# Performance work log

Measured on AMD Instinct MI355X. Metric: run time of the kernel, lower is better.

## Reference

```python
import jax, jax.numpy as jnp
import numpy as np

N_HEAD = 12

def setup_inputs() -> dict:
    key = jax.random.key(0)
    k1, k2, k3 = jax.random.split(key, 3)
    nx = 768
    B, S = 2, 2048
    return {
        "hidden_states": jax.random.normal(k1, (B, S, nx), dtype=jnp.float32),
        "w_attn": jax.random.normal(k2, (nx, 3 * nx), dtype=jnp.float32) * 0.02,
        "b_attn": jnp.zeros((3 * nx,), dtype=jnp.float32),
        "w_proj": jax.random.normal(k3, (nx, nx), dtype=jnp.float32) * 0.02,
        "b_proj": jnp.zeros((nx,), dtype=jnp.float32),
    }

def reference(hidden_states, w_attn, b_attn, w_proj, b_proj):
    B, S, nx = hidden_states.shape
    d_head = nx // N_HEAD
    qkv = hidden_states @ w_attn + b_attn  # [B,S,3nx]
    q, k, v = jnp.split(qkv, 3, axis=-1)
    # split heads -> [B,H,S,d]
    def split(x):
        return x.reshape(B, S, N_HEAD, d_head).transpose(0, 2, 1, 3)
    q, k, v = split(q), split(k), split(v)
    # scale=True: divide by sqrt(d_head) (v.size(-1))
    w = jnp.einsum("bhsd,bhtd->bhst", q, k) / jnp.sqrt(jnp.float32(d_head))
    w = jax.nn.softmax(w, axis=-1)
    a = jnp.einsum("bhst,bhtd->bhsd", w, v)  # [B,H,S,d]
    a = a.transpose(0, 2, 1, 3).reshape(B, S, nx)  # merge heads
    return a @ w_proj + b_proj
```

## Files before the change

kernel.cpp:

```cpp
#include <hip/hip_runtime.h>

#define NHEAD 12
#define DHEAD 64
#define SEQ   2048
#define NB    2
#define NX    768
#define MTOK  (NB * SEQ)

typedef __attribute__((ext_vector_type(8))) short short8;
typedef __attribute__((ext_vector_type(4))) short short4v;
typedef __attribute__((ext_vector_type(4))) float f32x4;

__device__ __forceinline__ unsigned short f2bf(float x) {
    union { float f; unsigned u; } v; v.f = x;
    unsigned r = v.u + 0x7fffu + ((v.u >> 16) & 1u);
    return (unsigned short)(r >> 16);
}

__device__ __forceinline__ float fexp2(float x) {
#if __has_builtin(__builtin_amdgcn_exp2f)
    return __builtin_amdgcn_exp2f(x);
#else
    float r; asm("v_exp_f32 %0, %1" : "=v"(r) : "v"(x)); return r;
#endif
}

#define MFMA32(a, b, c) __builtin_amdgcn_mfma_f32_16x16x32_bf16(a, b, c, 0, 0, 0)
#define MFMA16(a, b, c) __builtin_amdgcn_mfma_f32_16x16x16bf16_1k(a, b, c, 0, 0, 0)

__global__ __launch_bounds__(256)
void cvt_all(const float* __restrict__ hs,
             const float* __restrict__ wa, const float* __restrict__ wp,
             unsigned short* __restrict__ Abf,
             unsigned short* __restrict__ WtA, unsigned short* __restrict__ WtP)
{
    __shared__ float tile[32][33];
    const int bid = blockIdx.x;
    const int t = threadIdx.x;

    if (bid < 3072) {
        int i = bid * 256 + t;
        if (i >= 786432) return;
        float4 v = ((const float4*)hs)[i];
        ushort4 o;
        o.x = f2bf(v.x); o.y = f2bf(v.y); o.z = f2bf(v.z); o.w = f2bf(v.w);
        ((ushort4*)Abf)[i] = o;
        return;
    }

    const float* W; unsigned short* T; int K, N, bx, by;
    if (bid < 4800) {
        int b2 = bid - 3072;
        bx = b2 % 72; by = b2 / 72;
        W = wa; T = WtA; K = NX; N = 3 * NX;
    } else {
        int b2 = bid - 4800;
        bx = b2 % 24; by = b2 / 24;
        W = wp; T = WtP; K = NX; N = NX;
    }
    const int r = t >> 5, c = t & 31;
    const int k0 = by * 32, n0 = bx * 32;
#pragma unroll
    for (int i = 0; i < 4; i++)
        tile[r + i * 8][c] = W[(size_t)(k0 + r + i * 8) * N + n0 + c];
    __syncthreads();
#pragma unroll
    for (int i = 0; i < 4; i++) {
        int n = r + i * 8;
        T[(size_t)(n0 + n) * K + k0 + c] = f2bf(tile[c][n]);
    }
}

template<int MODE>
__global__ __launch_bounds__(256, 3)
void gemm_bf(const unsigned short* __restrict__ A,
             const unsigned short* __restrict__ Bt,
             const float* __restrict__ bias,
             float* __restrict__ fo,
             unsigned short* __restrict__ qb, unsigned short* __restrict__ kb2,
             unsigned short* __restrict__ vtb,
             int M, int N, int K)
{
    __shared__ __align__(16) unsigned char sm[2][16384];
    const int t = threadIdx.x;
    const int w = t >> 6, lane = t & 63;
    const int lo16 = lane & 15, quad = lane >> 4;
    const int ib = blockIdx.y * 128, jb = blockIdx.x * 128;

    f32x4 acc[4][4];
#pragma unroll
    for (int mt = 0; mt < 4; mt++)
#pragma unroll
        for (int nt = 0; nt < 4; nt++) acc[mt][nt] = (f32x4){0.f, 0.f, 0.f, 0.f};

    const int srow = lane >> 2;
    const int sj   = lane & 3;

    auto stage = [&](int buf, int k0) {
#pragma unroll
        for (int i = 0; i < 4; i++) {
            const int u   = i * 4 + w;
            const int p   = u >> 3;
            const int row = (u & 7) * 16 + srow;
            const int sc  = sj ^ (row & 3);
            const unsigned short* g = (p == 0)
                ? (A  + (size_t)(ib + row) * K + k0 + sc * 8)
                : (Bt + (size_t)(jb + row) * K + k0 + sc * 8);
            void* lp = &sm[buf][p * 8192 + (u & 7) * 1024];
            __builtin_amdgcn_global_load_lds(
                (const __attribute__((address_space(1))) unsigned int*)g,
                (__attribute__((address_space(3))) unsigned int*)lp, 16, 0, 0);
        }
    };

    const int mrow = (w >> 1) * 64;
    const int nrow = (w & 1) * 64;

    stage(0, 0);
    const int NIT = K / 32;
    for (int kt = 0; kt < NIT; kt++) {
        const int buf = kt & 1;
        __syncthreads();
        if (kt + 1 < NIT) stage(buf ^ 1, (kt + 1) * 32);

        short8 af[4], bf[4];
#pragma unroll
        for (int mt = 0; mt < 4; mt++) {
            const int row = mrow + mt * 16 + lo16;
            af[mt] = *(const short8*)&sm[buf][row * 64 + ((quad ^ (row & 3)) * 16)];
        }
#pragma unroll
        for (int nt = 0; nt < 4; nt++) {
            const int row = nrow + nt * 16 + lo16;
            bf[nt] = *(const short8*)&sm[buf][8192 + row * 64 + ((quad ^ (row & 3)) * 16)];
        }
#pragma unroll
        for (int mt = 0; mt < 4; mt++)
#pragma unroll
            for (int nt = 0; nt < 4; nt++)
                acc[mt][nt] = MFMA32(af[mt], bf[nt], acc[mt][nt]);
    }

    if constexpr (MODE == 0) {
        const int which = jb / NX;
#pragma unroll
        for (int nt = 0; nt < 4; nt++) {
            const int j  = jb + nrow + nt * 16 + lo16;
            const int cc = j - which * NX;
            const int hh = cc >> 6, dd = cc & 63;
            const float bj = bias[j];
#pragma unroll
            for (int mt = 0; mt < 4; mt++) {
                const int m0 = ib + mrow + mt * 16 + quad * 4;
                const int bb = m0 >> 11;
                const int s0 = m0 & 2047;
                const size_t hb = (size_t)(bb * NHEAD + hh);
                if (which == 2) {
                    ushort4 pv;
                    pv.x = f2bf(acc[mt][nt][0] + bj);
                    pv.y = f2bf(acc[mt][nt][1] + bj);
                    pv.z = f2bf(acc[mt][nt][2] + bj);
                    pv.w = f2bf(acc[mt][nt][3] + bj);
                    *(ushort4*)(vtb + (hb * DHEAD + dd) * SEQ + s0) = pv;
                } else {
                    unsigned short* dst = (which == 0) ? qb : kb2;
                    const float sc = (which == 0) ? 0.18033688011112042f : 1.0f;
#pragma unroll
                    for (int r = 0; r < 4; r++)
                        dst[(hb * SEQ + s0 + r) * DHEAD + dd] =
                            f2bf((acc[mt][nt][r] + bj) * sc);
                }
            }
        }
    } else {
#pragma unroll
        for (int nt = 0; nt < 4; nt++) {
            const int j  = jb + nrow + nt * 16 + lo16;
            const float bj = bias[j];
#pragma unroll
            for (int mt = 0; mt < 4; mt++) {
                const int m0 = ib + mrow + mt * 16 + quad * 4;
#pragma unroll
                for (int r = 0; r < 4; r++)
                    fo[(size_t)(m0 + r) * N + j] = acc[mt][nt][r] + bj;
            }
        }
    }
}

__global__ __launch_bounds__(256, 3)
void attn_bf(const unsigned short* __restrict__ qb, const unsigned short* __restrict__ kb,
             const unsigned short* __restrict__ vtb, unsigned short* __restrict__ ab)
{
    __shared__ __align__(16) unsigned char sm[2][16384];
    const int t = threadIdx.x;
    const int w = t >> 6, lane = t & 63;
    const int lo16 = lane & 15, quad = lane >> 4;

    const int id = blockIdx.x;
    const int xcd = id & 7, slot = id >> 3;
    const int bh = xcd * 3 + slot % 3;
    const int q0 = (slot / 3) * 64;
    const int b = bh / NHEAD, h = bh % NHEAD;

    const unsigned short* Qb = qb  + (size_t)bh * SEQ * DHEAD;
    const unsigned short* Kb = kb  + (size_t)bh * SEQ * DHEAD;
    const unsigned short* Vb = vtb + (size_t)bh * DHEAD * SEQ;

    short8 qf[2];
    {
        const size_t qo = (size_t)(q0 + w * 16 + lo16) * DHEAD + quad * 8;
        qf[0] = *(const short8*)(Qb + qo);
        qf[1] = *(const short8*)(Qb + qo + 32);
    }

    const int srow = lane >> 3;
    const int sj   = lane & 7;
    auto stage = [&](int buf, int k0) {
#pragma unroll
        for (int i = 0; i < 4; i++) {
            const int u   = i * 4 + w;
            const int p   = u >> 3;
            const int row = (u & 7) * 8 + srow;
            const int sc  = sj ^ (row & 7);
            const unsigned short* g = (p == 0)
                ? (Kb + (size_t)(k0 + row) * DHEAD + sc * 8)
                : (Vb + (size_t)row * SEQ + k0 + sc * 8);
            void* lp = &sm[buf][p * 8192 + (u & 7) * 1024];
            __builtin_amdgcn_global_load_lds(
                (const __attribute__((address_space(1))) unsigned int*)g,
                (__attribute__((address_space(3))) unsigned int*)lp, 16, 0, 0);
        }
    };

    f32x4 oacc[4];
#pragma unroll
    for (int dt = 0; dt < 4; dt++) oacc[dt] = (f32x4){0.f, 0.f, 0.f, 0.f};
    float lsum = 0.f;

    stage(0, 0);
    for (int kt = 0; kt < SEQ / 64; kt++) {
        const int buf = kt & 1;
        __syncthreads();
        if (kt + 1 < SEQ / 64) stage(buf ^ 1, (kt + 1) * 64);

        f32x4 s[4];
#pragma unroll
        for (int rt = 0; rt < 4; rt++) {
            const int row = rt * 16 + lo16;
            const int rs = row & 7;
            short8 kf0 = *(const short8*)&sm[buf][row * 128 + ((quad ^ rs) * 16)];
            short8 kf1 = *(const short8*)&sm[buf][row * 128 + (((4 + quad) ^ rs) * 16)];
            f32x4 a = (f32x4){0.f, 0.f, 0.f, 0.f};
            a = MFMA32(kf0, qf[0], a);
            a = MFMA32(kf1, qf[1], a);
            s[rt] = a;
        }

        short4v pf[4];
#pragma unroll
        for (int rt = 0; rt < 4; rt++) {
            float p0 = fexp2(s[rt][0]), p1 = fexp2(s[rt][1]);
            float p2 = fexp2(s[rt][2]), p3 = fexp2(s[rt][3]);
            lsum += (p0 + p1) + (p2 + p3);
            short4v pv;
            pv[0] = (short)f2bf(p0); pv[1] = (short)f2bf(p1);
            pv[2] = (short)f2bf(p2); pv[3] = (short)f2bf(p3);
            pf[rt] = pv;
        }

        __builtin_amdgcn_s_setprio(1);
#pragma unroll
        for (int dt = 0; dt < 4; dt++) {
            const int row = dt * 16 + lo16;
            const int rs = row & 7;
            f32x4 a = oacc[dt];
#pragma unroll
            for (int rt = 0; rt < 4; rt++) {
                const int ch = (2 * rt + (quad >> 1)) ^ rs;
                short4v vf = *(const short4v*)&sm[buf][8192 + row * 128 + ch * 16 + (quad & 1) * 8];
                a = MFMA16(vf, pf[rt], a);
            }
            oacc[dt] = a;
        }
        __builtin_amdgcn_s_setprio(0);
    }

    lsum += __shfl_xor(lsum, 16);
    lsum += __shfl_xor(lsum, 32);
    const float inv = 1.0f / lsum;

    unsigned short* dst = ab + (size_t)(b * SEQ + q0 + w * 16 + lo16) * NX + h * DHEAD;
#pragma unroll
    for (int dt = 0; dt < 4; dt++) {
        ushort4 pv;
        pv.x = f2bf(oacc[dt][0] * inv);
        pv.y = f2bf(oacc[dt][1] * inv);
        pv.z = f2bf(oacc[dt][2] * inv);
        pv.w = f2bf(oacc[dt][3] * inv);
        *(ushort4*)(dst + dt * 16 + quad * 4) = pv;
    }
}

extern "C" void kernel_launch(void* const* d_in, const int* in_sizes, int n_in,
                              void* d_out, int out_size, void* d_ws, size_t ws_size,
                              hipStream_t stream)
{
    const float* hs     = (const float*)d_in[0];
    const float* w_attn = (const float*)d_in[1];
    const float* b_attn = (const float*)d_in[2];
    const float* w_proj = (const float*)d_in[3];
    const float* b_proj = (const float*)d_in[4];
    float* out = (float*)d_out;

    unsigned short* wsu = (unsigned short*)d_ws;
    unsigned short* Abf  = wsu;
    unsigned short* WtA  = Abf  + 3145728;
    unsigned short* WtP  = WtA  + 1769472;
    unsigned short* qbuf = WtP  + 589824;
    unsigned short* kbuf = qbuf + 3145728;
    unsigned short* vtbf = kbuf + 3145728;
    unsigned short* abf  = vtbf + 3145728;

    cvt_all<<<5376, 256, 0, stream>>>(hs, w_attn, w_proj, Abf, WtA, WtP);

    gemm_bf<0><<<dim3(18, 32), 256, 0, stream>>>(
        Abf, WtA, b_attn, nullptr, qbuf, kbuf, vtbf, MTOK, 3 * NX, NX);

    attn_bf<<<768, 256, 0, stream>>>(qbuf, kbuf, vtbf, abf);

    gemm_bf<1><<<dim3(6, 32), 256, 0, stream>>>(
        abf, WtP, b_proj, out, nullptr, nullptr, nullptr, MTOK, NX, NX);
}
```

Measured before the change: 161.8 us.

## Give each attention wave two query tiles to reuse K/V fragments

The attention kernel now uses 2 waves of 128 threads per block, each handling 32 query rows (two 16-row tiles) instead of 16. Every K and V fragment read from LDS then feeds two MFMA chains, halving LDS reads per unit of compute and giving more independent MFMAs per wave. The tradeoff is higher register pressure and fewer waves per block, which cuts latency hiding and raises the per-wave staging work. The launch bounds hint is lowered to 2.

Result: slower. 179.1 us (+10.7%).

```diff
diff --git a/kernel.cpp b/kernel.cpp
--- a/kernel.cpp
+++ b/kernel.cpp
@@ -188,7 +188,7 @@
     }
 }
 
-__global__ __launch_bounds__(256, 3)
+__global__ __launch_bounds__(128, 2)
 void attn_bf(const unsigned short* __restrict__ qb, const unsigned short* __restrict__ kb,
              const unsigned short* __restrict__ vtb, unsigned short* __restrict__ ab)
 {
@@ -207,19 +207,20 @@
     const unsigned short* Kb = kb  + (size_t)bh * SEQ * DHEAD;
     const unsigned short* Vb = vtb + (size_t)bh * DHEAD * SEQ;
 
-    short8 qf[2];
-    {
-        const size_t qo = (size_t)(q0 + w * 16 + lo16) * DHEAD + quad * 8;
-        qf[0] = *(const short8*)(Qb + qo);
-        qf[1] = *(const short8*)(Qb + qo + 32);
+    short8 qf[2][2];
+#pragma unroll
+    for (int qt = 0; qt < 2; qt++) {
+        const size_t qo = (size_t)(q0 + w * 32 + qt * 16 + lo16) * DHEAD + quad * 8;
+        qf[qt][0] = *(const short8*)(Qb + qo);
+        qf[qt][1] = *(const short8*)(Qb + qo + 32);
     }
 
     const int srow = lane >> 3;
     const int sj   = lane & 7;
     auto stage = [&](int buf, int k0) {
 #pragma unroll
-        for (int i = 0; i < 4; i++) {
-            const int u   = i * 4 + w;
+        for (int i = 0; i < 8; i++) {
+            const int u   = i * 2 + w;
             const int p   = u >> 3;
             const int row = (u & 7) * 8 + srow;
             const int sc  = sj ^ (row & 7);
@@ -233,10 +234,12 @@
         }
     };
 
-    f32x4 oacc[4];
-#pragma unroll
-    for (int dt = 0; dt < 4; dt++) oacc[dt] = (f32x4){0.f, 0.f, 0.f, 0.f};
-    float lsum = 0.f;
+    f32x4 oacc[2][4];
+#pragma unroll
+    for (int qt = 0; qt < 2; qt++)
+#pragma unroll
+        for (int dt = 0; dt < 4; dt++) oacc[qt][dt] = (f32x4){0.f, 0.f, 0.f, 0.f};
+    float lsum[2] = {0.f, 0.f};
 
     stage(0, 0);
     for (int kt = 0; kt < SEQ / 64; kt++) {
@@ -244,29 +247,26 @@
         __syncthreads();
         if (kt + 1 < SEQ / 64) stage(buf ^ 1, (kt + 1) * 64);
 
-        f32x4 s[4];
+        short4v pf[2][4];
 #pragma unroll
         for (int rt = 0; rt < 4; rt++) {
             const int row = rt * 16 + lo16;
             const int rs = row & 7;
             short8 kf0 = *(const short8*)&sm[buf][row * 128 + ((quad ^ rs) * 16)];
             short8 kf1 = *(const short8*)&sm[buf][row * 128 + (((4 + quad) ^ rs) * 16)];
-            f32x4 a = (f32x4){0.f, 0.f, 0.f, 0.f};
-            a = MFMA32(kf0, qf[0], a);
-            a = MFMA32(kf1, qf[1], a);
-            s[rt] = a;
-        }
-
-        short4v pf[4];
-#pragma unroll
-        for (int rt = 0; rt < 4; rt++) {
-            float p0 = fexp2(s[rt][0]), p1 = fexp2(s[rt][1]);
-            float p2 = fexp2(s[rt][2]), p3 = fexp2(s[rt][3]);
-            lsum += (p0 + p1) + (p2 + p3);
-            short4v pv;
-            pv[0] = (short)f2bf(p0); pv[1] = (short)f2bf(p1);
-            pv[2] = (short)f2bf(p2); pv[3] = (short)f2bf(p3);
-            pf[rt] = pv;
+#pragma unroll
+            for (int qt = 0; qt < 2; qt++) {
+                f32x4 a = (f32x4){0.f, 0.f, 0.f, 0.f};
+                a = MFMA32(kf0, qf[qt][0], a);
+                a = MFMA32(kf1, qf[qt][1], a);
+                float p0 = fexp2(a[0]), p1 = fexp2(a[1]);
+                float p2 = fexp2(a[2]), p3 = fexp2(a[3]);
+                lsum[qt] += (p0 + p1) + (p2 + p3);
+                short4v pv;
+                pv[0] = (short)f2bf(p0); pv[1] = (short)f2bf(p1);
+                pv[2] = (short)f2bf(p2); pv[3] = (short)f2bf(p3);
+                pf[qt][rt] = pv;
+            }
         }
 
         __builtin_amdgcn_s_setprio(1);
@@ -274,31 +274,36 @@
         for (int dt = 0; dt < 4; dt++) {
             const int row = dt * 16 + lo16;
             const int rs = row & 7;
-            f32x4 a = oacc[dt];
+            f32x4 a0 = oacc[0][dt], a1 = oacc[1][dt];
 #pragma unroll
             for (int rt = 0; rt < 4; rt++) {
                 const int ch = (2 * rt + (quad >> 1)) ^ rs;
                 short4v vf = *(const short4v*)&sm[buf][8192 + row * 128 + ch * 16 + (quad & 1) * 8];
-                a = MFMA16(vf, pf[rt], a);
+                a0 = MFMA16(vf, pf[0][rt], a0);
+                a1 = MFMA16(vf, pf[1][rt], a1);
             }
-            oacc[dt] = a;
+            oacc[0][dt] = a0; oacc[1][dt] = a1;
         }
         __builtin_amdgcn_s_setprio(0);
     }
 
-    lsum += __shfl_xor(lsum, 16);
-    lsum += __shfl_xor(lsum, 32);
-    const float inv = 1.0f / lsum;
-
-    unsigned short* dst = ab + (size_t)(b * SEQ + q0 + w * 16 + lo16) * NX + h * DHEAD;
-#pragma unroll
-    for (int dt = 0; dt < 4; dt++) {
-        ushort4 pv;
-        pv.x = f2bf(oacc[dt][0] * inv);
-        pv.y = f2bf(oacc[dt][1] * inv);
-        pv.z = f2bf(oacc[dt][2] * inv);
-        pv.w = f2bf(oacc[dt][3] * inv);
-        *(ushort4*)(dst + dt * 16 + quad * 4) = pv;
+#pragma unroll
+    for (int qt = 0; qt < 2; qt++) {
+        lsum[qt] += __shfl_xor(lsum[qt], 16);
+        lsum[qt] += __shfl_xor(lsum[qt], 32);
+        const float inv = 1.0f / lsum[qt];
+
+        unsigned short* dst =
+            ab + (size_t)(b * SEQ + q0 + w * 32 + qt * 16 + lo16) * NX + h * DHEAD;
+#pragma unroll
+        for (int dt = 0; dt < 4; dt++) {
+            ushort4 pv;
+            pv.x = f2bf(oacc[qt][dt][0] * inv);
+            pv.y = f2bf(oacc[qt][dt][1] * inv);
+            pv.z = f2bf(oacc[qt][dt][2] * inv);
+            pv.w = f2bf(oacc[qt][dt][3] * inv);
+            *(ushort4*)(dst + dt * 16 + quad * 4) = pv;
+        }
     }
 }
 
@@ -327,7 +332,7 @@
     gemm_bf<0><<<dim3(18, 32), 256, 0, stream>>>(
         Abf, WtA, b_attn, nullptr, qbuf, kbuf, vtbf, MTOK, 3 * NX, NX);
 
-    attn_bf<<<768, 256, 0, stream>>>(qbuf, kbuf, vtbf, abf);
+    attn_bf<<<768, 128, 0, stream>>>(qbuf, kbuf, vtbf, abf);
 
     gemm_bf<1><<<dim3(6, 32), 256, 0, stream>>>(
         abf, WtP, b_proj, out, nullptr, nullptr, nullptr, MTOK, NX, NX);
```

## Load V fragments directly from global into registers and swizzle GEMM block order

Applied to the files above, without the earlier changes.

The attention kernel no longer stages V^T tiles through LDS. Each lane now loads its V fragments straight from global memory into registers every iteration, which halves LDS use and the async-copy work. Each wave therefore issues its own redundant global loads of V, and their latency is exposed within the same iteration rather than prefetched a stage ahead. Separately, the GEMM remaps workgroup ids so that consecutive blocks are spread across the 8 XCDs, aiming for better L2 locality.

Result: slower. 298.6 us (+84.5%).

```diff
diff --git a/kernel.cpp b/kernel.cpp
--- a/kernel.cpp
+++ b/kernel.cpp
@@ -85,7 +85,11 @@
     const int t = threadIdx.x;
     const int w = t >> 6, lane = t & 63;
     const int lo16 = lane & 15, quad = lane >> 4;
-    const int ib = blockIdx.y * 128, jb = blockIdx.x * 128;
+
+    const int nwg  = gridDim.x * gridDim.y;
+    const int flat = blockIdx.y * gridDim.x + blockIdx.x;
+    const int swz  = (flat & 7) * (nwg >> 3) + (flat >> 3);
+    const int ib = (swz / gridDim.x) * 128, jb = (swz % gridDim.x) * 128;
 
     f32x4 acc[4][4];
 #pragma unroll
@@ -192,7 +196,7 @@
 void attn_bf(const unsigned short* __restrict__ qb, const unsigned short* __restrict__ kb,
              const unsigned short* __restrict__ vtb, unsigned short* __restrict__ ab)
 {
-    __shared__ __align__(16) unsigned char sm[2][16384];
+    __shared__ __align__(16) unsigned char sm[2][8192];
     const int t = threadIdx.x;
     const int w = t >> 6, lane = t & 63;
     const int lo16 = lane & 15, quad = lane >> 4;
@@ -214,19 +218,18 @@
         qf[1] = *(const short8*)(Qb + qo + 32);
     }
 
+    const unsigned short* Vl = Vb + (size_t)lo16 * SEQ + quad * 4;
+
     const int srow = lane >> 3;
     const int sj   = lane & 7;
     auto stage = [&](int buf, int k0) {
 #pragma unroll
-        for (int i = 0; i < 4; i++) {
+        for (int i = 0; i < 2; i++) {
             const int u   = i * 4 + w;
-            const int p   = u >> 3;
-            const int row = (u & 7) * 8 + srow;
+            const int row = u * 8 + srow;
             const int sc  = sj ^ (row & 7);
-            const unsigned short* g = (p == 0)
-                ? (Kb + (size_t)(k0 + row) * DHEAD + sc * 8)
-                : (Vb + (size_t)row * SEQ + k0 + sc * 8);
-            void* lp = &sm[buf][p * 8192 + (u & 7) * 1024];
+            const unsigned short* g = Kb + (size_t)(k0 + row) * DHEAD + sc * 8;
+            void* lp = &sm[buf][u * 1024];
             __builtin_amdgcn_global_load_lds(
                 (const __attribute__((address_space(1))) unsigned int*)g,
                 (__attribute__((address_space(3))) unsigned int*)lp, 16, 0, 0);
@@ -243,6 +246,14 @@
         const int buf = kt & 1;
         __syncthreads();
         if (kt + 1 < SEQ / 64) stage(buf ^ 1, (kt + 1) * 64);
+
+        short4v vreg[4][4];
+#pragma unroll
+        for (int dt = 0; dt < 4; dt++)
+#pragma unroll
+            for (int rt = 0; rt < 4; rt++)
+                vreg[dt][rt] = *(const short4v*)
+                    (Vl + (size_t)dt * 16 * SEQ + kt * 64 + rt * 16);
 
         f32x4 s[4];
 #pragma unroll
@@ -272,15 +283,10 @@
         __builtin_amdgcn_s_setprio(1);
 #pragma unroll
         for (int dt = 0; dt < 4; dt++) {
-            const int row = dt * 16 + lo16;
-            const int rs = row & 7;
             f32x4 a = oacc[dt];
 #pragma unroll
-            for (int rt = 0; rt < 4; rt++) {
-                const int ch = (2 * rt + (quad >> 1)) ^ rs;
-                short4v vf = *(const short4v*)&sm[buf][8192 + row * 128 + ch * 16 + (quad & 1) * 8];
-                a = MFMA16(vf, pf[rt], a);
-            }
+            for (int rt = 0; rt < 4; rt++)
+                a = MFMA16(vreg[dt][rt], pf[rt], a);
             oacc[dt] = a;
         }
         __builtin_amdgcn_s_setprio(0);
```

## Use 16x16x32 MFMA for PV via permuted K rows; swizzle GEMM block order

Applied to the files above, without the earlier changes.

The attention kernel loads K rows into LDS in a permuted order so that the S tile's output layout directly forms 8-element P fragments. The P·V product can then use the wider 16x16x32 bf16 MFMA with 16-byte V reads, replacing four 16x16x16 MFMAs with two. Separately, the GEMM remaps workgroup IDs with a stride-8 swizzle to change which tiles run together and improve cache locality. The K permutation must stay consistent with the V column ordering, or the results will be wrong.

New measurement: 151.9 us. 1.07x faster.

```diff
diff --git a/kernel.cpp b/kernel.cpp
--- a/kernel.cpp
+++ b/kernel.cpp
@@ -26,7 +26,6 @@
 }
 
 #define MFMA32(a, b, c) __builtin_amdgcn_mfma_f32_16x16x32_bf16(a, b, c, 0, 0, 0)
-#define MFMA16(a, b, c) __builtin_amdgcn_mfma_f32_16x16x16bf16_1k(a, b, c, 0, 0, 0)
 
 __global__ __launch_bounds__(256)
 void cvt_all(const float* __restrict__ hs,
@@ -85,7 +84,11 @@
     const int t = threadIdx.x;
     const int w = t >> 6, lane = t & 63;
     const int lo16 = lane & 15, quad = lane >> 4;
-    const int ib = blockIdx.y * 128, jb = blockIdx.x * 128;
+
+    const int nwg  = gridDim.x * gridDim.y;
+    const int flat = blockIdx.y * gridDim.x + blockIdx.x;
+    const int swz  = (flat & 7) * (nwg >> 3) + (flat >> 3);
+    const int ib = (swz / gridDim.x) * 128, jb = (swz % gridDim.x) * 128;
 
     f32x4 acc[4][4];
 #pragma unroll
@@ -223,8 +226,10 @@
             const int p   = u >> 3;
             const int row = (u & 7) * 8 + srow;
             const int sc  = sj ^ (row & 7);
+            const int gr  = (row & 32) | (((row >> 2) & 3) << 3)
+                          | (((row >> 4) & 1) << 2) | (row & 3);
             const unsigned short* g = (p == 0)
-                ? (Kb + (size_t)(k0 + row) * DHEAD + sc * 8)
+                ? (Kb + (size_t)(k0 + gr) * DHEAD + sc * 8)
                 : (Vb + (size_t)row * SEQ + k0 + sc * 8);
             void* lp = &sm[buf][p * 8192 + (u & 7) * 1024];
             __builtin_amdgcn_global_load_lds(
@@ -257,16 +262,19 @@
             s[rt] = a;
         }
 
-        short4v pf[4];
-#pragma unroll
-        for (int rt = 0; rt < 4; rt++) {
-            float p0 = fexp2(s[rt][0]), p1 = fexp2(s[rt][1]);
-            float p2 = fexp2(s[rt][2]), p3 = fexp2(s[rt][3]);
-            lsum += (p0 + p1) + (p2 + p3);
-            short4v pv;
-            pv[0] = (short)f2bf(p0); pv[1] = (short)f2bf(p1);
-            pv[2] = (short)f2bf(p2); pv[3] = (short)f2bf(p3);
-            pf[rt] = pv;
+        short8 pf[2];
+#pragma unroll
+        for (int f = 0; f < 2; f++) {
+            short8 pv;
+#pragma unroll
+            for (int r = 0; r < 4; r++) {
+                float p0 = fexp2(s[2 * f][r]);
+                float p1 = fexp2(s[2 * f + 1][r]);
+                lsum += p0 + p1;
+                pv[r]     = (short)f2bf(p0);
+                pv[4 + r] = (short)f2bf(p1);
+            }
+            pf[f] = pv;
         }
 
         __builtin_amdgcn_s_setprio(1);
@@ -274,13 +282,11 @@
         for (int dt = 0; dt < 4; dt++) {
             const int row = dt * 16 + lo16;
             const int rs = row & 7;
+            short8 vf0 = *(const short8*)&sm[buf][8192 + row * 128 + ((quad ^ rs) * 16)];
+            short8 vf1 = *(const short8*)&sm[buf][8192 + row * 128 + (((4 + quad) ^ rs) * 16)];
             f32x4 a = oacc[dt];
-#pragma unroll
-            for (int rt = 0; rt < 4; rt++) {
-                const int ch = (2 * rt + (quad >> 1)) ^ rs;
-                short4v vf = *(const short4v*)&sm[buf][8192 + row * 128 + ch * 16 + (quad & 1) * 8];
-                a = MFMA16(vf, pf[rt], a);
-            }
+            a = MFMA32(vf0, pf[0], a);
+            a = MFMA32(vf1, pf[1], a);
             oacc[dt] = a;
         }
         __builtin_amdgcn_s_setprio(0);
```
